# Kernel optimization log

Hardware: AMD Instinct MI355X
Metric: run time of the kernel (lower is better)

## Reference

```python
import jax, jax.numpy as jnp
import numpy as np

H = 4  # heads
L = 2  # num_layers


def _segment_softmax(alpha, seg, num_segments):
    # alpha: [E, H], seg: [E] destination node ids
    m = jax.ops.segment_max(alpha, seg, num_segments=num_segments)  # [N, H]
    m = jnp.where(jnp.isfinite(m), m, 0.0)
    ex = jnp.exp(alpha - m[seg])
    s = jax.ops.segment_sum(ex, seg, num_segments=num_segments)  # [N, H]
    return ex / (s[seg] + 1e-16)


def _conv(x, src, dst, edge_weight, edge_attr, wq, wk, wv, we, g, b):
    # x: [N, D]; edge_attr: [E, D]; one WePredConv layer (eval mode, no dropout)
    N, D = x.shape
    C = D // H
    q = (x @ wq).reshape(N, H, C)
    k = (x @ wk).reshape(N, H, C)
    v = (x @ wv).reshape(N, H, C)
    e = (edge_attr @ we).reshape(-1, H, C)
    alpha = (q[dst] + k[src] + e).sum(-1) / jnp.sqrt(jnp.float32(C))  # [E, H]
    alpha = alpha + g[None, :] * edge_weight[:, None]
    alpha = jax.nn.leaky_relu(alpha, negative_slope=0.2)
    alpha = _segment_softmax(alpha, dst, N)
    msg = v[src] * alpha[:, :, None]  # [E, H, C]
    out = jax.ops.segment_sum(msg, dst, num_segments=N).reshape(N, H * C)
    return out + b


def setup_inputs() -> dict:
    key = jax.random.key(0)
    ks = jax.random.split(key, 12)
    N, E, D, F, R = 50000, 400000, 128, 256, 200
    sc = 0.08  # ~xavier scale
    return {
        "entity": jnp.arange(N, dtype=jnp.int32),
        "edge_index": jax.random.randint(ks[0], (2, E), 0, N, dtype=jnp.int32),
        "edge_type": jax.random.randint(ks[1], (E,), 0, R, dtype=jnp.int32),
        "edge_weight": jax.random.uniform(ks[2], (E,), dtype=jnp.float32),
        "ent_table": jax.random.normal(ks[3], (N, F), dtype=jnp.float32),
        "proj_w": jax.random.normal(ks[4], (F, D), dtype=jnp.float32) * sc,
        "proj_b": jnp.zeros((D,), dtype=jnp.float32),
        "rel_emb": jax.random.normal(ks[5], (R, D), dtype=jnp.float32) * sc,
        "Wq": jax.random.normal(ks[6], (L, D, D), dtype=jnp.float32) * sc,
        "Wk": jax.random.normal(ks[7], (L, D, D), dtype=jnp.float32) * sc,
        "Wv": jax.random.normal(ks[8], (L, D, D), dtype=jnp.float32) * sc,
        "We": jax.random.normal(ks[9], (L, D, D), dtype=jnp.float32) * sc,
        "gate": jnp.ones((L, H), dtype=jnp.float32),
        "conv_bias": jnp.zeros((L, D), dtype=jnp.float32),
    }


def reference(entity, edge_index, edge_type, edge_weight, ent_table, proj_w,
              proj_b, rel_emb, Wq, Wk, Wv, We, gate, conv_bias):
    src, dst = edge_index[0], edge_index[1]
    x = ent_table[entity] @ proj_w + proj_b          # [N, D]
    edge_attr = rel_emb[edge_type]                   # [E, D]
    for l in range(L):
        x = _conv(x, src, dst, edge_weight, edge_attr,
                  Wq[l], Wk[l], Wv[l], We[l], gate[l], conv_bias[l])
        if l != L - 1:
            x = jax.nn.elu(x)
    return x
```

## Files before the change

### kernel.cpp

```cpp
#include <hip/hip_runtime.h>
#include <hip/hip_fp16.h>

#define HD 4
#define DD 128
#define CC 32
#define SCAN_B 64
#define SCAN_T 256

typedef float  f32x4   __attribute__((ext_vector_type(4)));
typedef short  short8v __attribute__((ext_vector_type(8)));

__device__ __forceinline__ unsigned short f2bf(float x) {
    unsigned u = __float_as_uint(x);
    return (unsigned short)((u + 0x7FFFu + ((u >> 16) & 1u)) >> 16);
}
__device__ __forceinline__ float bf2f(unsigned short h) {
    return __uint_as_float((unsigned)h << 16);
}

__global__ __launch_bounds__(256) void prep_kernel(
    const float* __restrict__ Wq, const float* __restrict__ Wk,
    const float* __restrict__ We, const float* __restrict__ rel,
    float* __restrict__ Wqh, float* __restrict__ Wkh,
    float* __restrict__ esum, int R)
{
    __shared__ float WehS[2][DD][HD];
    int tid = threadIdx.x;
    for (int i = tid; i < 2 * DD * HD; i += 256) {
        int l = i / (DD * HD);
        int d = (i / HD) % DD;
        int h = i % HD;
        const float* bq = Wq + ((size_t)l * DD + d) * DD + h * CC;
        const float* bk = Wk + ((size_t)l * DD + d) * DD + h * CC;
        const float* be = We + ((size_t)l * DD + d) * DD + h * CC;
        float sq = 0.f, sk = 0.f, se = 0.f;
        for (int c = 0; c < CC; ++c) { sq += bq[c]; sk += bk[c]; se += be[c]; }
        Wqh[i] = sq; Wkh[i] = sk; WehS[l][d][h] = se;
    }
    __syncthreads();
    for (int i = tid; i < 2 * R * HD; i += 256) {
        int l = i / (R * HD);
        int r = (i / HD) % R;
        int h = i % HD;
        const float* rp = rel + (size_t)r * DD;
        float a = 0.f;
        for (int d = 0; d < DD; ++d) a += rp[d] * WehS[l][d][h];
        esum[i] = a;
    }
}

__global__ __launch_bounds__(256) void prep_bt(
    const float* __restrict__ pw, const float* __restrict__ Wv,
    unsigned short* __restrict__ btp, unsigned short* __restrict__ btv)
{
    int t = blockIdx.x * 256 + threadIdx.x;
    if (t < 128 * 256) {
        int col = t >> 8, k = t & 255;
        btp[(size_t)col * 256 + k] = f2bf(pw[(size_t)k * DD + col]);
    } else if (t < 128 * 256 + 2 * DD * DD) {
        int u = t - 128 * 256;
        int l = u >> 14;
        int r = u & 16383;
        int col = r >> 7, k = r & 127;
        btv[((size_t)l * DD + col) * DD + k] = f2bf(Wv[((size_t)l * DD + k) * DD + col]);
    }
}

__global__ __launch_bounds__(256) void gemm_mfma(
    const float* __restrict__ A, const int* __restrict__ gather,
    const unsigned short* __restrict__ bth, const float* __restrict__ bias,
    const float* __restrict__ Wqh, const float* __restrict__ Wkh,
    float* __restrict__ Cf, __half* __restrict__ Chf,
    float* __restrict__ qs, float* __restrict__ ks,
    int M, int K)
{
    __shared__ unsigned short AhL[4][4][64][8];
    __shared__ unsigned short AlL[4][4][64][8];
    __shared__ unsigned short BhL[4][8][64][8];
    __shared__ float wq[DD * HD], wk[DD * HD];

    const int tid = threadIdx.x;
    const int wave = tid >> 6, lane = tid & 63;
    const int row0 = blockIdx.x * 64;

    if (qs) {
        for (int i = tid; i < DD * HD; i += 256) { wq[i] = Wqh[i]; wk[i] = Wkh[i]; }
    }

    const int sr = tid >> 2;
    const int sks = tid & 3;
    int arow = row0 + sr; if (arow >= M) arow = M - 1;
    const int ga = gather ? gather[arow] : arow;
    const float* Ap = A + (size_t)ga * K + sks * 32;

    const int bc = tid >> 1;
    const int bh2 = (tid & 1) * 64;
    const unsigned short* Bp = bth + (size_t)bc * K + bh2;
    const int bct = bc >> 4, bfr = bc & 15;

    const int fr = lane & 15, fg = lane >> 4;

    f32x4 acc[8] = {};
    float qp[4] = {}, kp[4] = {};

    const int nch = K >> 7;
    for (int ch = 0; ch < nch; ++ch) {
        float4 a[8];
#pragma unroll
        for (int i = 0; i < 8; ++i) a[i] = *(const float4*)(Ap + ch * 128 + i * 4);
        short8v b[8];
#pragma unroll
        for (int i = 0; i < 8; ++i) b[i] = *(const short8v*)(Bp + ch * 128 + i * 8);

        if (ch) __syncthreads();

        {
            const int rt = sr >> 4, frr = sr & 15;
#pragma unroll
            for (int g = 0; g < 4; ++g) {
                float vv[8] = {a[g*2].x, a[g*2].y, a[g*2].z, a[g*2].w,
                               a[g*2+1].x, a[g*2+1].y, a[g*2+1].z, a[g*2+1].w};
                short8v hv, lv;
#pragma unroll
                for (int j = 0; j < 8; ++j) {
                    unsigned short h = f2bf(vv[j]);
                    hv[j] = (short)h;
                    lv[j] = (short)f2bf(vv[j] - bf2f(h));
                }
                *(short8v*)&AhL[rt][sks][g * 16 + frr][0] = hv;
                *(short8v*)&AlL[rt][sks][g * 16 + frr][0] = lv;
            }
        }
        if (qs) {
#pragma unroll
            for (int i = 0; i < 8; ++i) {
                const float arr[4] = {a[i].x, a[i].y, a[i].z, a[i].w};
#pragma unroll
                for (int j = 0; j < 4; ++j) {
                    int d = ch * 128 + sks * 32 + i * 4 + j;
                    float4 qw = *(const float4*)&wq[d * HD];
                    float4 kw = *(const float4*)&wk[d * HD];
                    qp[0] += arr[j] * qw.x; qp[1] += arr[j] * qw.y;
                    qp[2] += arr[j] * qw.z; qp[3] += arr[j] * qw.w;
                    kp[0] += arr[j] * kw.x; kp[1] += arr[j] * kw.y;
                    kp[2] += arr[j] * kw.z; kp[3] += arr[j] * kw.w;
                }
            }
        }
#pragma unroll
        for (int g = 0; g < 8; ++g) {
            int kk = bh2 + g * 8;
            int ksb = kk >> 5, fgb = (kk & 31) >> 3;
            *(short8v*)&BhL[ksb][bct][fgb * 16 + bfr][0] = b[g];
        }
        __syncthreads();

#pragma unroll
        for (int ksc = 0; ksc < 4; ++ksc) {
            short8v ah = *(const short8v*)&AhL[wave][ksc][lane][0];
            short8v al = *(const short8v*)&AlL[wave][ksc][lane][0];
#pragma unroll
            for (int c = 0; c < 8; ++c) {
                short8v bh = *(const short8v*)&BhL[ksc][c][lane][0];
                acc[c] = __builtin_amdgcn_mfma_f32_16x16x32_bf16(ah, bh, acc[c], 0, 0, 0);
                acc[c] = __builtin_amdgcn_mfma_f32_16x16x32_bf16(al, bh, acc[c], 0, 0, 0);
            }
        }
    }

    if (qs) {
#pragma unroll
        for (int off = 1; off < 4; off <<= 1) {
#pragma unroll
            for (int h = 0; h < 4; ++h) {
                qp[h] += __shfl_xor(qp[h], off, 64);
                kp[h] += __shfl_xor(kp[h], off, 64);
            }
        }
        if ((tid & 3) == 0) {
            int row = row0 + sr;
            if (row < M) {
                *(float4*)&qs[(size_t)row * HD] = make_float4(qp[0], qp[1], qp[2], qp[3]);
                *(float4*)&ks[(size_t)row * HD] = make_float4(kp[0], kp[1], kp[2], kp[3]);
            }
        }
    }

#pragma unroll
    for (int c = 0; c < 8; ++c) {
        float bv = bias ? bias[c * 16 + fr] : 0.f;
#pragma unroll
        for (int i = 0; i < 4; ++i) {
            int row = row0 + wave * 16 + fg * 4 + i;
            if (row < M) {
                float val = acc[c][i] + bv;
                if (Chf) Chf[(size_t)row * DD + c * 16 + fr] = __float2half(val);
                else     Cf [(size_t)row * DD + c * 16 + fr] = val;
            }
        }
    }
}

__global__ __launch_bounds__(256) void csr_count(
    const int* __restrict__ dstv, int* __restrict__ deg, int E)
{
    int t = blockIdx.x * 256 + threadIdx.x;
    if (t < E) atomicAdd(&deg[dstv[t]], 1);
}

__global__ __launch_bounds__(SCAN_T) void scan_partial(
    const int* __restrict__ deg, int* __restrict__ blksum, int N)
{
    __shared__ int red[SCAN_T];
    int chunk = (N + SCAN_B - 1) / SCAN_B;
    int b0 = blockIdx.x * chunk;
    int e0 = b0 + chunk; if (e0 > N) e0 = N;
    int s = 0;
    for (int i = b0 + threadIdx.x; i < e0; i += SCAN_T) s += deg[i];
    red[threadIdx.x] = s;
    __syncthreads();
    for (int off = SCAN_T / 2; off > 0; off >>= 1) {
        if (threadIdx.x < off) red[threadIdx.x] += red[threadIdx.x + off];
        __syncthreads();
    }
    if (threadIdx.x == 0) blksum[blockIdx.x] = red[0];
}

__global__ __launch_bounds__(64) void scan_blk(
    const int* __restrict__ blksum, int* __restrict__ blkoff)
{
    if (threadIdx.x == 0) {
        int acc = 0;
        for (int i = 0; i < SCAN_B; ++i) { blkoff[i] = acc; acc += blksum[i]; }
        blkoff[SCAN_B] = acc;
    }
}

__global__ __launch_bounds__(SCAN_T) void scan_final(
    const int* __restrict__ deg, const int* __restrict__ blkoff,
    int* __restrict__ row_ptr, int N)
{
    __shared__ int tsum[SCAN_T];
    int tid = threadIdx.x;
    int chunk = (N + SCAN_B - 1) / SCAN_B;
    int b0 = blockIdx.x * chunk;
    int e0 = b0 + chunk; if (e0 > N) e0 = N;
    int tchunk = (chunk + SCAN_T - 1) / SCAN_T;
    int tb = b0 + tid * tchunk;
    int te = tb + tchunk; if (te > e0) te = e0;
    int s = 0;
    for (int i = tb; i < te; ++i) s += deg[i];
    tsum[tid] = s;
    __syncthreads();
    for (int off = 1; off < SCAN_T; off <<= 1) {
        int v = (tid >= off) ? tsum[tid - off] : 0;
        __syncthreads();
        tsum[tid] += v;
        __syncthreads();
    }
    int base = blkoff[blockIdx.x] + ((tid == 0) ? 0 : tsum[tid - 1]);
    for (int i = tb; i < te; ++i) { row_ptr[i] = base; base += deg[i]; }
    if (blockIdx.x == SCAN_B - 1 && tid == SCAN_T - 1) row_ptr[N] = blkoff[SCAN_B];
}

__global__ __launch_bounds__(256) void csr_scatter(
    const int* __restrict__ srcv, const int* __restrict__ dstv,
    const int* __restrict__ etype, const float* __restrict__ ew,
    const int* __restrict__ row_ptr, int* __restrict__ cursor,
    int4* __restrict__ c_pack, int E)
{
    int e = blockIdx.x * 256 + threadIdx.x;
    if (e >= E) return;
    int d = dstv[e];
    int p = row_ptr[d] + atomicAdd(&cursor[d], 1);
    c_pack[p] = make_int4(srcv[e], etype[e], __float_as_int(ew[e]), 0);
}

__global__ __launch_bounds__(256) void fused_conv(
    const int* __restrict__ row_ptr, const int4* __restrict__ c_pack,
    const float* __restrict__ qs, const float* __restrict__ ks,
    const float* __restrict__ esum, const float* __restrict__ gate,
    const __half* __restrict__ v, const float* __restrict__ bias,
    float* __restrict__ out, int N, int do_elu)
{
    int gw = (blockIdx.x * 256 + threadIdx.x) >> 6;
    int lane = threadIdx.x & 63;
    if (gw >= N) return;
    const int n = gw;
    const int beg = row_ptr[n], end = row_ptr[n + 1];
    const int c0 = lane * 2;
    const int h = lane >> 4;
    const float L2E = 1.4426950408889634f;
    const float scL = 0.17677669529663687f * 1.4426950408889634f;
    const float qh = qs[(size_t)n * HD + h];
    const float ghL = gate[h] * L2E;

    float num0 = 0.f, num1 = 0.f, den = 0.f;

    int j = beg;
    for (; j + 4 <= end; j += 4) {
        int4 p0 = c_pack[j];
        int4 p1 = c_pack[j + 1];
        int4 p2 = c_pack[j + 2];
        int4 p3 = c_pack[j + 3];
        float kh0 = ks[(size_t)p0.x * HD + h];
        float kh1 = ks[(size_t)p1.x * HD + h];
        float kh2 = ks[(size_t)p2.x * HD + h];
        float kh3 = ks[(size_t)p3.x * HD + h];
        float eh0 = esum[(size_t)p0.y * HD + h];
        float eh1 = esum[(size_t)p1.y * HD + h];
        float eh2 = esum[(size_t)p2.y * HD + h];
        float eh3 = esum[(size_t)p3.y * HD + h];
        float2 vv0 = __half22float2(*(const __half2*)&v[(size_t)p0.x * DD + c0]);
        float2 vv1 = __half22float2(*(const __half2*)&v[(size_t)p1.x * DD + c0]);
        float2 vv2 = __half22float2(*(const __half2*)&v[(size_t)p2.x * DD + c0]);
        float2 vv3 = __half22float2(*(const __half2*)&v[(size_t)p3.x * DD + c0]);
        float a0 = (qh + kh0 + eh0) * scL + ghL * __int_as_float(p0.z);
        float a1 = (qh + kh1 + eh1) * scL + ghL * __int_as_float(p1.z);
        float a2 = (qh + kh2 + eh2) * scL + ghL * __int_as_float(p2.z);
        float a3 = (qh + kh3 + eh3) * scL + ghL * __int_as_float(p3.z);
        a0 = a0 > 0.f ? a0 : 0.2f * a0;
        a1 = a1 > 0.f ? a1 : 0.2f * a1;
        a2 = a2 > 0.f ? a2 : 0.2f * a2;
        a3 = a3 > 0.f ? a3 : 0.2f * a3;
        float e0 = exp2f(a0), e1 = exp2f(a1);
        float e2 = exp2f(a2), e3 = exp2f(a3);
        den += (e0 + e1) + (e2 + e3);
        num0 = fmaf(e0, vv0.x, num0); num1 = fmaf(e0, vv0.y, num1);
        num0 = fmaf(e1, vv1.x, num0); num1 = fmaf(e1, vv1.y, num1);
        num0 = fmaf(e2, vv2.x, num0); num1 = fmaf(e2, vv2.y, num1);
        num0 = fmaf(e3, vv3.x, num0); num1 = fmaf(e3, vv3.y, num1);
    }
    for (; j < end; ++j) {
        int4 cur = c_pack[j];
        float kh = ks[(size_t)cur.x * HD + h];
        float eh = esum[(size_t)cur.y * HD + h];
        float2 vv = __half22float2(*(const __half2*)&v[(size_t)cur.x * DD + c0]);
        float a = (qh + kh + eh) * scL + ghL * __int_as_float(cur.z);
        a = a > 0.f ? a : 0.2f * a;
        float e = exp2f(a);
        den += e;
        num0 = fmaf(e, vv.x, num0);
        num1 = fmaf(e, vv.y, num1);
    }

    float inv = 1.f / (den + 1e-16f);
    float r0 = num0 * inv + bias[c0];
    float r1 = num1 * inv + bias[c0 + 1];
    if (do_elu) {
        r0 = r0 > 0.f ? r0 : expm1f(r0);
        r1 = r1 > 0.f ? r1 : expm1f(r1);
    }
    *(float2*)&out[(size_t)n * DD + c0] = make_float2(r0, r1);
}

extern "C" void kernel_launch(void* const* d_in, const int* in_sizes, int n_in,
                              void* d_out, int out_size, void* d_ws, size_t ws_size,
                              hipStream_t stream)
{
    const int*   entity = (const int*)d_in[0];
    const int*   eidx   = (const int*)d_in[1];
    const int*   etype  = (const int*)d_in[2];
    const float* ew     = (const float*)d_in[3];
    const float* ent    = (const float*)d_in[4];
    const float* pw     = (const float*)d_in[5];
    const float* pb     = (const float*)d_in[6];
    const float* rel    = (const float*)d_in[7];
    const float* Wq     = (const float*)d_in[8];
    const float* Wk     = (const float*)d_in[9];
    const float* Wv     = (const float*)d_in[10];
    const float* We     = (const float*)d_in[11];
    const float* gate   = (const float*)d_in[12];
    const float* cb     = (const float*)d_in[13];

    const int N = in_sizes[0];
    const int E = in_sizes[2];
    const int F = in_sizes[4] / N;
    const int R = in_sizes[7] / DD;

    const int* srcv = eidx;
    const int* dstv = eidx + E;

    float* ws = (float*)d_ws;
    size_t o = 0;
    float* xbuf    = ws + o; o += (size_t)N * DD;
    __half* vbuf   = (__half*)(ws + o); o += (size_t)N * DD / 2;
    float* qs      = ws + o; o += (size_t)N * HD;
    float* ks      = ws + o; o += (size_t)N * HD;
    float* Wqh     = ws + o; o += 2 * DD * HD;
    float* Wkh     = ws + o; o += 2 * DD * HD;
    float* esum    = ws + o; o += (size_t)2 * R * HD;
    int*   deg     = (int*)(ws + o); o += N;
    int*   cursor  = (int*)(ws + o); o += N;
    int*   row_ptr = (int*)(ws + o); o += (size_t)N + 1;
    int*   blksum  = (int*)(ws + o); o += SCAN_B;
    int*   blkoff  = (int*)(ws + o); o += SCAN_B + 1;
    o = (o + 3) & ~(size_t)3;
    int4*  c_pack  = (int4*)(ws + o); o += (size_t)E * 4;
    unsigned short* btp = (unsigned short*)(ws + o); o += 128 * 256 / 2;
    unsigned short* btv = (unsigned short*)(ws + o); o += 2 * DD * DD / 2;

    prep_kernel<<<1, 256, 0, stream>>>(Wq, Wk, We, rel, Wqh, Wkh, esum, R);
    prep_bt<<<(128 * 256 + 2 * DD * DD + 255) / 256, 256, 0, stream>>>(
        pw, Wv, btp, btv);

    hipMemsetAsync(deg, 0, (size_t)2 * N * sizeof(int), stream);
    csr_count<<<(E + 255) / 256, 256, 0, stream>>>(dstv, deg, E);
    scan_partial<<<SCAN_B, SCAN_T, 0, stream>>>(deg, blksum, N);
    scan_blk<<<1, 64, 0, stream>>>(blksum, blkoff);
    scan_final<<<SCAN_B, SCAN_T, 0, stream>>>(deg, blkoff, row_ptr, N);
    csr_scatter<<<(E + 255) / 256, 256, 0, stream>>>(
        srcv, dstv, etype, ew, row_ptr, cursor, c_pack, E);

    const int gblk = (N + 63) / 64;
    gemm_mfma<<<gblk, 256, 0, stream>>>(
        ent, entity, btp, pb, nullptr, nullptr,
        xbuf, nullptr, nullptr, nullptr, N, F);

    const int fblk = (N + 3) / 4;
    for (int l = 0; l < 2; ++l) {
        gemm_mfma<<<gblk, 256, 0, stream>>>(
            xbuf, nullptr, btv + (size_t)l * DD * DD, nullptr,
            Wqh + l * DD * HD, Wkh + l * DD * HD,
            nullptr, vbuf, qs, ks, N, DD);
        fused_conv<<<fblk, 256, 0, stream>>>(
            row_ptr, c_pack, qs, ks, esum + (size_t)l * R * HD,
            gate + l * HD, vbuf, cb + l * DD,
            (l == 0) ? xbuf : (float*)d_out, N, (l == 0) ? 1 : 0);
    }
}
```

Baseline: 234.6 us.

## Parallelize prep kernel, read GEMM B directly from global, unroll edge loop by 8

Three changes. The weight-prep kernel now runs on 16 blocks, with each block recomputing the small head sums and splitting the relation-embedding projection across the grid. The MFMA GEMM drops its LDS staging of B and loads B fragments straight from global memory (L1/L2) inside the inner loop, which removes LDS writes and pressure but issues more global loads per MFMA. The edge-aggregation kernel gains an 8-wide unrolled loop so more gathers are in flight per wave, at the cost of higher register use.

```diff
diff --git a/kernel.cpp b/kernel.cpp
--- a/kernel.cpp
+++ b/kernel.cpp
@@ -35,10 +35,11 @@
         const float* be = We + ((size_t)l * DD + d) * DD + h * CC;
         float sq = 0.f, sk = 0.f, se = 0.f;
         for (int c = 0; c < CC; ++c) { sq += bq[c]; sk += bk[c]; se += be[c]; }
-        Wqh[i] = sq; Wkh[i] = sk; WehS[l][d][h] = se;
+        if (blockIdx.x == 0) { Wqh[i] = sq; Wkh[i] = sk; }
+        WehS[l][d][h] = se;
     }
     __syncthreads();
-    for (int i = tid; i < 2 * R * HD; i += 256) {
+    for (int i = blockIdx.x * 256 + tid; i < 2 * R * HD; i += gridDim.x * 256) {
         int l = i / (R * HD);
         int r = (i / HD) % R;
         int h = i % HD;
@@ -76,7 +77,6 @@
 {
     __shared__ unsigned short AhL[4][4][64][8];
     __shared__ unsigned short AlL[4][4][64][8];
-    __shared__ unsigned short BhL[4][8][64][8];
     __shared__ float wq[DD * HD], wk[DD * HD];
 
     const int tid = threadIdx.x;
@@ -93,12 +93,8 @@
     const int ga = gather ? gather[arow] : arow;
     const float* Ap = A + (size_t)ga * K + sks * 32;
 
-    const int bc = tid >> 1;
-    const int bh2 = (tid & 1) * 64;
-    const unsigned short* Bp = bth + (size_t)bc * K + bh2;
-    const int bct = bc >> 4, bfr = bc & 15;
-
     const int fr = lane & 15, fg = lane >> 4;
+    const unsigned short* Bb = bth + (size_t)fr * K + fg * 8;
 
     f32x4 acc[8] = {};
     float qp[4] = {}, kp[4] = {};
@@ -108,9 +104,6 @@
         float4 a[8];
 #pragma unroll
         for (int i = 0; i < 8; ++i) a[i] = *(const float4*)(Ap + ch * 128 + i * 4);
-        short8v b[8];
-#pragma unroll
-        for (int i = 0; i < 8; ++i) b[i] = *(const short8v*)(Bp + ch * 128 + i * 8);
 
         if (ch) __syncthreads();
 
@@ -147,23 +140,20 @@
                 }
             }
         }
-#pragma unroll
-        for (int g = 0; g < 8; ++g) {
-            int kk = bh2 + g * 8;
-            int ksb = kk >> 5, fgb = (kk & 31) >> 3;
-            *(short8v*)&BhL[ksb][bct][fgb * 16 + bfr][0] = b[g];
-        }
         __syncthreads();
 
 #pragma unroll
         for (int ksc = 0; ksc < 4; ++ksc) {
             short8v ah = *(const short8v*)&AhL[wave][ksc][lane][0];
             short8v al = *(const short8v*)&AlL[wave][ksc][lane][0];
+            short8v bhv[8];
+#pragma unroll
+            for (int c = 0; c < 8; ++c)
+                bhv[c] = *(const short8v*)(Bb + (size_t)(c * 16) * K + ch * 128 + ksc * 32);
 #pragma unroll
             for (int c = 0; c < 8; ++c) {
-                short8v bh = *(const short8v*)&BhL[ksc][c][lane][0];
-                acc[c] = __builtin_amdgcn_mfma_f32_16x16x32_bf16(ah, bh, acc[c], 0, 0, 0);
-                acc[c] = __builtin_amdgcn_mfma_f32_16x16x32_bf16(al, bh, acc[c], 0, 0, 0);
+                acc[c] = __builtin_amdgcn_mfma_f32_16x16x32_bf16(ah, bhv[c], acc[c], 0, 0, 0);
+                acc[c] = __builtin_amdgcn_mfma_f32_16x16x32_bf16(al, bhv[c], acc[c], 0, 0, 0);
             }
         }
     }
@@ -298,6 +288,29 @@
     float num0 = 0.f, num1 = 0.f, den = 0.f;
 
     int j = beg;
+    for (; j + 8 <= end; j += 8) {
+        int4 p[8];
+#pragma unroll
+        for (int u = 0; u < 8; ++u) p[u] = c_pack[j + u];
+        float kh[8], eh[8];
+        float2 vv[8];
+#pragma unroll
+        for (int u = 0; u < 8; ++u) kh[u] = ks[(size_t)p[u].x * HD + h];
+#pragma unroll
+        for (int u = 0; u < 8; ++u) eh[u] = esum[(size_t)p[u].y * HD + h];
+#pragma unroll
+        for (int u = 0; u < 8; ++u)
+            vv[u] = __half22float2(*(const __half2*)&v[(size_t)p[u].x * DD + c0]);
+#pragma unroll
+        for (int u = 0; u < 8; ++u) {
+            float a = (qh + kh[u] + eh[u]) * scL + ghL * __int_as_float(p[u].z);
+            a = a > 0.f ? a : 0.2f * a;
+            float e = exp2f(a);
+            den += e;
+            num0 = fmaf(e, vv[u].x, num0);
+            num1 = fmaf(e, vv[u].y, num1);
+        }
+    }
     for (; j + 4 <= end; j += 4) {
         int4 p0 = c_pack[j];
         int4 p1 = c_pack[j + 1];
@@ -400,7 +413,7 @@
     unsigned short* btp = (unsigned short*)(ws + o); o += 128 * 256 / 2;
     unsigned short* btv = (unsigned short*)(ws + o); o += 2 * DD * DD / 2;
 
-    prep_kernel<<<1, 256, 0, stream>>>(Wq, Wk, We, rel, Wqh, Wkh, esum, R);
+    prep_kernel<<<16, 256, 0, stream>>>(Wq, Wk, We, rel, Wqh, Wkh, esum, R);
     prep_bt<<<(128 * 256 + 2 * DD * DD + 255) / 256, 256, 0, stream>>>(
         pw, Wv, btp, btv);
 
```

Result: slower. 271.1 us (+15.6%).
